# Performance work log

Measured on AMD Instinct MI355X. Metric: run time of the kernel, lower is better.

The kernel has to match this reference:

```python
import jax, jax.numpy as jnp
import numpy as np

# The torch module expresses conv as unfold -> linear (no bias) -> fold(1x1).
# That pipeline is mathematically exactly a VALID cross-correlation with the
# Linear weight reshaped to OIHW (torch unfold flattens patches in (C, kh, kw)
# order, matching Linear's in_features layout). We implement it as the
# efficient direct conv, which computes identical math.

B = 2048

def setup_inputs() -> dict:
    key = jax.random.key(0)
    k1, k2, k3 = jax.random.split(key, 3)
    x = jax.random.normal(k1, (B, 784), dtype=jnp.float32)
    # nn.Linear(49 -> 10, bias=False) and nn.Linear(250 -> 10, bias=False)
    W1 = jax.random.normal(k2, (10, 49), dtype=jnp.float32) * (1.0 / np.sqrt(49.0))
    W2 = jax.random.normal(k3, (10, 250), dtype=jnp.float32) * (1.0 / np.sqrt(250.0))
    return {"x": x, "W1": W1, "W2": W2}

def _conv(x, w_oihw):
    return jax.lax.conv_general_dilated(
        x, w_oihw, window_strides=(1, 1), padding='VALID',
        dimension_numbers=('NCHW', 'OIHW', 'NCHW'))

def _relu_ratio(x_base):
    # x = relu(x_base); ratio = x / x_base with NaN/Inf -> 0 (matches
    # calculate_ratio: 0/0 -> NaN -> 0, relu(neg)/neg -> -0 -> stays 0)
    x = jax.nn.relu(x_base)
    rat = x / x_base
    rat = jnp.where(jnp.isnan(rat) | jnp.isinf(rat), jnp.float32(0.0), rat)
    return x, rat

def reference(x, W1, W2):
    b = x.shape[0]
    h = x.reshape(b, 1, 28, 28)
    # layer 1: unfold(7x7) + linear(49->10) + fold == conv, out (b,10,22,22)
    h = _conv(h, W1.reshape(10, 1, 7, 7))
    h, rat1 = _relu_ratio(h)
    # layer 2: unfold(5x5) + linear(250->10) + fold == conv, out (b,10,18,18)
    h = _conv(h, W2.reshape(10, 10, 5, 5))
    h, rat2 = _relu_ratio(h)
    return (h, rat1, rat2)
```

## Files before the change

### kernel.cpp

```cpp
#include <hip/hip_runtime.h>


#define THREADS 256

__global__ __launch_bounds__(THREADS, 4) void brewcnn_v6(
    const float* __restrict__ x,
    const float* __restrict__ Wa,
    const float* __restrict__ Wb,
    float* __restrict__ out,
    int nimg)
{
    __shared__ __align__(16) float s_x[784];
    __shared__ __align__(16) float s_h[10 * 532];
    __shared__ __align__(16) float s_wa[492];
    __shared__ __align__(16) float s_wb[2840];
    const int img = blockIdx.x;
    const int tid = threadIdx.x;

    if (tid < 196)
        reinterpret_cast<float4*>(s_x)[tid] =
            reinterpret_cast<const float4*>(x + img * 784)[tid];
    if (tid < 122)
        reinterpret_cast<float4*>(s_wa)[tid] =
            reinterpret_cast<const float4*>(Wa)[tid];
    if (tid == 196) { s_wa[488] = Wa[488]; s_wa[489] = Wa[489]; }
    for (int t = tid; t < 2500; t += THREADS) {
        const int oc  = t / 250;
        const int rem = t - oc * 250;
        const int ic  = rem / 25;
        const int k   = rem - ic * 25;
        s_wb[oc * 284 + ic * 28 + k] = Wb[t];
    }
    __syncthreads();

    const int h2_base = img * 3240;
    const int r1_base = nimg * 3240 + img * 4840;
    const int r2_base = nimg * 8080 + img * 3240;

    {
        const int t   = tid < 220 ? tid : 219;
        const int row = t / 10;
        const int oc  = t - row * 10;

        float acc[22];
#pragma unroll
        for (int i = 0; i < 22; ++i) acc[i] = 0.0f;

        const float* wrow = s_wa + oc * 49;
#pragma unroll 1
        for (int ky = 0; ky < 7; ++ky) {
            float in[28];
            const float4* rp = reinterpret_cast<const float4*>(s_x + (row + ky) * 28);
#pragma unroll
            for (int j = 0; j < 7; ++j) {
                const float4 v = rp[j];
                in[4*j+0] = v.x; in[4*j+1] = v.y; in[4*j+2] = v.z; in[4*j+3] = v.w;
            }
            float w[7];
#pragma unroll
            for (int k = 0; k < 7; ++k) w[k] = wrow[ky * 7 + k];
#pragma unroll
            for (int kx = 0; kx < 7; ++kx)
#pragma unroll
                for (int px = 0; px < 22; ++px)
                    acc[px] = fmaf(in[px + kx], w[kx], acc[px]);
        }

        float r1v[22];
#pragma unroll
        for (int px = 0; px < 22; ++px) {
            const float h = acc[px];
            acc[px] = h > 0.0f ? h : 0.0f;
            r1v[px] = h > 0.0f ? 1.0f : 0.0f;
        }
        float* hdst = s_h + oc * 532 + row * 24;
#pragma unroll
        for (int j = 0; j < 5; ++j)
            reinterpret_cast<float4*>(hdst)[j] =
                make_float4(acc[4*j], acc[4*j+1], acc[4*j+2], acc[4*j+3]);
        hdst[20] = acc[20];
        hdst[21] = acc[21];

        float* r1p = out + r1_base + oc * 484 + row * 22;
#pragma unroll
        for (int j = 0; j < 11; ++j)
            reinterpret_cast<float2*>(r1p)[j] = make_float2(r1v[2*j], r1v[2*j+1]);
    }
    __syncthreads();

    {
        const int t   = tid < 180 ? tid : 179;
        const int row = t / 10;
        const int oc  = t - row * 10;

        float acc[18];
#pragma unroll
        for (int i = 0; i < 18; ++i) acc[i] = 0.0f;

#pragma unroll 1
        for (int ic = 0; ic < 10; ++ic) {
            float w[28];
            const float4* wp = reinterpret_cast<const float4*>(s_wb + oc * 284 + ic * 28);
#pragma unroll
            for (int j = 0; j < 7; ++j) {
                const float4 v = wp[j];
                w[4*j+0] = v.x; w[4*j+1] = v.y; w[4*j+2] = v.z; w[4*j+3] = v.w;
            }
            const float* hb = s_h + ic * 532 + row * 24;
#pragma unroll
            for (int ky = 0; ky < 5; ++ky) {
                float in[24];
                const float4* rp = reinterpret_cast<const float4*>(hb + ky * 24);
#pragma unroll
                for (int j = 0; j < 6; ++j) {
                    const float4 v = rp[j];
                    in[4*j+0] = v.x; in[4*j+1] = v.y; in[4*j+2] = v.z; in[4*j+3] = v.w;
                }
#pragma unroll
                for (int kx = 0; kx < 5; ++kx)
#pragma unroll
                    for (int px = 0; px < 18; ++px)
                        acc[px] = fmaf(in[px + kx], w[ky * 5 + kx], acc[px]);
            }
        }

        float hv[18], rv[18];
#pragma unroll
        for (int px = 0; px < 18; ++px) {
            const float h = acc[px];
            hv[px] = h > 0.0f ? h : 0.0f;
            rv[px] = h > 0.0f ? 1.0f : 0.0f;
        }
        float* h2p = out + h2_base + oc * 324 + row * 18;
        float* r2p = out + r2_base + oc * 324 + row * 18;
#pragma unroll
        for (int j = 0; j < 9; ++j) {
            reinterpret_cast<float2*>(h2p)[j] = make_float2(hv[2*j], hv[2*j+1]);
            reinterpret_cast<float2*>(r2p)[j] = make_float2(rv[2*j], rv[2*j+1]);
        }
    }
}

extern "C" void kernel_launch(void* const* d_in, const int* in_sizes, int n_in,
                              void* d_out, int out_size, void* d_ws, size_t ws_size,
                              hipStream_t stream) {
    const float* x  = (const float*)d_in[0];
    const float* Wa = (const float*)d_in[1];
    const float* Wb = (const float*)d_in[2];
    float* out = (float*)d_out;
    const int nimg = in_sizes[0] / 784;

    brewcnn_v6<<<nimg, THREADS, 0, stream>>>(x, Wa, Wb, out, nimg);
}
```

Baseline: 179.7 us.

## Compute multiple output rows per thread to reuse input rows across conv layers

```diff
diff --git a/kernel.cpp b/kernel.cpp
--- a/kernel.cpp
+++ b/kernel.cpp
@@ -1,9 +1,9 @@
 #include <hip/hip_runtime.h>
 
 
-#define THREADS 256
-
-__global__ __launch_bounds__(THREADS, 4) void brewcnn_v6(
+#define THREADS 128
+
+__global__ __launch_bounds__(THREADS) void brewcnn_v7(
     const float* __restrict__ x,
     const float* __restrict__ Wa,
     const float* __restrict__ Wb,
@@ -12,24 +12,21 @@
 {
     __shared__ __align__(16) float s_x[784];
     __shared__ __align__(16) float s_h[10 * 532];
-    __shared__ __align__(16) float s_wa[492];
-    __shared__ __align__(16) float s_wb[2840];
+    __shared__ __align__(16) float s_wa[560];
+    __shared__ __align__(16) float s_wb[2800];
     const int img = blockIdx.x;
     const int tid = threadIdx.x;
 
-    if (tid < 196)
-        reinterpret_cast<float4*>(s_x)[tid] =
-            reinterpret_cast<const float4*>(x + img * 784)[tid];
-    if (tid < 122)
-        reinterpret_cast<float4*>(s_wa)[tid] =
-            reinterpret_cast<const float4*>(Wa)[tid];
-    if (tid == 196) { s_wa[488] = Wa[488]; s_wa[489] = Wa[489]; }
-    for (int t = tid; t < 2500; t += THREADS) {
-        const int oc  = t / 250;
-        const int rem = t - oc * 250;
-        const int ic  = rem / 25;
-        const int k   = rem - ic * 25;
-        s_wb[oc * 284 + ic * 28 + k] = Wb[t];
+    for (int i = tid; i < 196; i += THREADS)
+        reinterpret_cast<float4*>(s_x)[i] =
+            reinterpret_cast<const float4*>(x + img * 784)[i];
+    for (int i = tid; i < 560; i += THREADS) {
+        const int oc = i / 56, r = i - oc * 56, ky = r >> 3, k = r & 7;
+        s_wa[i] = (k < 7) ? Wa[oc * 49 + ky * 7 + k] : 0.0f;
+    }
+    for (int i = tid; i < 2800; i += THREADS) {
+        const int oc = i / 280, r = i - oc * 280, ic = r / 28, k = r - ic * 28;
+        s_wb[i] = (k < 25) ? Wb[oc * 250 + ic * 25 + k] : 0.0f;
     }
     __syncthreads();
 
@@ -38,105 +35,171 @@
     const int r2_base = nimg * 8080 + img * 3240;
 
     {
-        const int t   = tid < 220 ? tid : 219;
-        const int row = t / 10;
-        const int oc  = t - row * 10;
-
-        float acc[22];
-#pragma unroll
-        for (int i = 0; i < 22; ++i) acc[i] = 0.0f;
-
-        const float* wrow = s_wa + oc * 49;
-#pragma unroll 1
-        for (int ky = 0; ky < 7; ++ky) {
-            float in[28];
-            const float4* rp = reinterpret_cast<const float4*>(s_x + (row + ky) * 28);
+        const int t  = tid < 110 ? tid : 109;
+        const int g  = t / 10;
+        const int oc = t - g * 10;
+        const int r0 = 2 * g;
+
+        float acc[2][22];
+#pragma unroll
+        for (int o = 0; o < 2; ++o)
+#pragma unroll
+            for (int px = 0; px < 22; ++px) acc[o][px] = 0.0f;
+
+        float wcur[7], wprev[7];
+        float in[28];
+
+        {
+            const float4* rp = reinterpret_cast<const float4*>(s_x + r0 * 28);
 #pragma unroll
             for (int j = 0; j < 7; ++j) {
                 const float4 v = rp[j];
                 in[4*j+0] = v.x; in[4*j+1] = v.y; in[4*j+2] = v.z; in[4*j+3] = v.w;
             }
-            float w[7];
-#pragma unroll
-            for (int k = 0; k < 7; ++k) w[k] = wrow[ky * 7 + k];
+            const float4* wp = reinterpret_cast<const float4*>(s_wa + oc * 56);
+            const float4 a = wp[0], b = wp[1];
+            wcur[0]=a.x; wcur[1]=a.y; wcur[2]=a.z; wcur[3]=a.w;
+            wcur[4]=b.x; wcur[5]=b.y; wcur[6]=b.z;
 #pragma unroll
             for (int kx = 0; kx < 7; ++kx)
 #pragma unroll
                 for (int px = 0; px < 22; ++px)
-                    acc[px] = fmaf(in[px + kx], w[kx], acc[px]);
-        }
-
-        float r1v[22];
-#pragma unroll
-        for (int px = 0; px < 22; ++px) {
-            const float h = acc[px];
-            acc[px] = h > 0.0f ? h : 0.0f;
-            r1v[px] = h > 0.0f ? 1.0f : 0.0f;
-        }
-        float* hdst = s_h + oc * 532 + row * 24;
+                    acc[0][px] = fmaf(in[px + kx], wcur[kx], acc[0][px]);
+#pragma unroll
+            for (int k = 0; k < 7; ++k) wprev[k] = wcur[k];
+        }
+
+#pragma unroll 1
+        for (int ri = 1; ri <= 6; ++ri) {
+            const float4* rp = reinterpret_cast<const float4*>(s_x + (r0 + ri) * 28);
+#pragma unroll
+            for (int j = 0; j < 7; ++j) {
+                const float4 v = rp[j];
+                in[4*j+0] = v.x; in[4*j+1] = v.y; in[4*j+2] = v.z; in[4*j+3] = v.w;
+            }
+            const float4* wp = reinterpret_cast<const float4*>(s_wa + oc * 56 + ri * 8);
+            const float4 a = wp[0], b = wp[1];
+            wcur[0]=a.x; wcur[1]=a.y; wcur[2]=a.z; wcur[3]=a.w;
+            wcur[4]=b.x; wcur[5]=b.y; wcur[6]=b.z;
+#pragma unroll
+            for (int kx = 0; kx < 7; ++kx)
+#pragma unroll
+                for (int px = 0; px < 22; ++px) {
+                    acc[0][px] = fmaf(in[px + kx], wcur[kx], acc[0][px]);
+                    acc[1][px] = fmaf(in[px + kx], wprev[kx], acc[1][px]);
+                }
+#pragma unroll
+            for (int k = 0; k < 7; ++k) wprev[k] = wcur[k];
+        }
+
+        {
+            const float4* rp = reinterpret_cast<const float4*>(s_x + (r0 + 7) * 28);
+#pragma unroll
+            for (int j = 0; j < 7; ++j) {
+                const float4 v = rp[j];
+                in[4*j+0] = v.x; in[4*j+1] = v.y; in[4*j+2] = v.z; in[4*j+3] = v.w;
+            }
+#pragma unroll
+            for (int kx = 0; kx < 7; ++kx)
+#pragma unroll
+                for (int px = 0; px < 22; ++px)
+                    acc[1][px] = fmaf(in[px + kx], wprev[kx], acc[1][px]);
+        }
+
+        float h[2][22], r[2][22];
+#pragma unroll
+        for (int o = 0; o < 2; ++o)
+#pragma unroll
+            for (int px = 0; px < 22; ++px) {
+                const float v = acc[o][px];
+                h[o][px] = v > 0.0f ? v : 0.0f;
+                r[o][px] = v > 0.0f ? 1.0f : 0.0f;
+            }
+        float4* hd = reinterpret_cast<float4*>(s_h + oc * 532 + r0 * 24);
 #pragma unroll
         for (int j = 0; j < 5; ++j)
-            reinterpret_cast<float4*>(hdst)[j] =
-                make_float4(acc[4*j], acc[4*j+1], acc[4*j+2], acc[4*j+3]);
-        hdst[20] = acc[20];
-        hdst[21] = acc[21];
-
-        float* r1p = out + r1_base + oc * 484 + row * 22;
-#pragma unroll
-        for (int j = 0; j < 11; ++j)
-            reinterpret_cast<float2*>(r1p)[j] = make_float2(r1v[2*j], r1v[2*j+1]);
+            hd[j] = make_float4(h[0][4*j], h[0][4*j+1], h[0][4*j+2], h[0][4*j+3]);
+        hd[5] = make_float4(h[0][20], h[0][21], 0.0f, 0.0f);
+#pragma unroll
+        for (int j = 0; j < 5; ++j)
+            hd[6 + j] = make_float4(h[1][4*j], h[1][4*j+1], h[1][4*j+2], h[1][4*j+3]);
+        hd[11] = make_float4(h[1][20], h[1][21], 0.0f, 0.0f);
+
+        float4* rp1 = reinterpret_cast<float4*>(out + r1_base + oc * 484 + r0 * 22);
+#pragma unroll
+        for (int j = 0; j < 11; ++j) {
+            const int base = 4 * j;
+            float v[4];
+#pragma unroll
+            for (int q = 0; q < 4; ++q) {
+                const int idx = base + q;
+                v[q] = (idx < 22) ? r[0][idx] : r[1][idx - 22];
+            }
+            rp1[j] = make_float4(v[0], v[1], v[2], v[3]);
+        }
     }
     __syncthreads();
 
-    {
-        const int t   = tid < 180 ? tid : 179;
-        const int row = t / 10;
-        const int oc  = t - row * 10;
-
-        float acc[18];
-#pragma unroll
-        for (int i = 0; i < 18; ++i) acc[i] = 0.0f;
+    if (tid < 64) {
+        const int t  = tid < 60 ? tid : 59;
+        const int g  = t / 10;
+        const int oc = t - g * 10;
+        const int r0 = 3 * g;
+
+        float acc[3][18];
+#pragma unroll
+        for (int o = 0; o < 3; ++o)
+#pragma unroll
+            for (int px = 0; px < 18; ++px) acc[o][px] = 0.0f;
 
 #pragma unroll 1
         for (int ic = 0; ic < 10; ++ic) {
             float w[28];
-            const float4* wp = reinterpret_cast<const float4*>(s_wb + oc * 284 + ic * 28);
+            const float4* wp = reinterpret_cast<const float4*>(s_wb + oc * 280 + ic * 28);
 #pragma unroll
             for (int j = 0; j < 7; ++j) {
                 const float4 v = wp[j];
                 w[4*j+0] = v.x; w[4*j+1] = v.y; w[4*j+2] = v.z; w[4*j+3] = v.w;
             }
-            const float* hb = s_h + ic * 532 + row * 24;
-#pragma unroll
-            for (int ky = 0; ky < 5; ++ky) {
+            const float* hb = s_h + ic * 532 + r0 * 24;
+#pragma unroll
+            for (int ri = 0; ri < 7; ++ri) {
                 float in[24];
-                const float4* rp = reinterpret_cast<const float4*>(hb + ky * 24);
+                const float4* rp = reinterpret_cast<const float4*>(hb + ri * 24);
 #pragma unroll
                 for (int j = 0; j < 6; ++j) {
                     const float4 v = rp[j];
                     in[4*j+0] = v.x; in[4*j+1] = v.y; in[4*j+2] = v.z; in[4*j+3] = v.w;
                 }
 #pragma unroll
-                for (int kx = 0; kx < 5; ++kx)
-#pragma unroll
-                    for (int px = 0; px < 18; ++px)
-                        acc[px] = fmaf(in[px + kx], w[ky * 5 + kx], acc[px]);
-            }
-        }
-
-        float hv[18], rv[18];
-#pragma unroll
-        for (int px = 0; px < 18; ++px) {
-            const float h = acc[px];
-            hv[px] = h > 0.0f ? h : 0.0f;
-            rv[px] = h > 0.0f ? 1.0f : 0.0f;
-        }
-        float* h2p = out + h2_base + oc * 324 + row * 18;
-        float* r2p = out + r2_base + oc * 324 + row * 18;
-#pragma unroll
-        for (int j = 0; j < 9; ++j) {
-            reinterpret_cast<float2*>(h2p)[j] = make_float2(hv[2*j], hv[2*j+1]);
-            reinterpret_cast<float2*>(r2p)[j] = make_float2(rv[2*j], rv[2*j+1]);
+                for (int o = 0; o < 3; ++o) {
+                    const int ky = ri - o;
+                    if (ky >= 0 && ky <= 4) {
+#pragma unroll
+                        for (int kx = 0; kx < 5; ++kx)
+#pragma unroll
+                            for (int px = 0; px < 18; ++px)
+                                acc[o][px] = fmaf(in[px + kx], w[ky * 5 + kx], acc[o][px]);
+                    }
+                }
+            }
+        }
+
+        float hv[54], rv[54];
+#pragma unroll
+        for (int o = 0; o < 3; ++o)
+#pragma unroll
+            for (int px = 0; px < 18; ++px) {
+                const float v = acc[o][px];
+                hv[o * 18 + px] = v > 0.0f ? v : 0.0f;
+                rv[o * 18 + px] = v > 0.0f ? 1.0f : 0.0f;
+            }
+        float2* h2p = reinterpret_cast<float2*>(out + h2_base + oc * 324 + r0 * 18);
+        float2* r2p = reinterpret_cast<float2*>(out + r2_base + oc * 324 + r0 * 18);
+#pragma unroll
+        for (int j = 0; j < 27; ++j) {
+            h2p[j] = make_float2(hv[2*j], hv[2*j+1]);
+            r2p[j] = make_float2(rv[2*j], rv[2*j+1]);
         }
     }
 }
@@ -150,5 +213,5 @@
     float* out = (float*)d_out;
     const int nimg = in_sizes[0] / 784;
 
-    brewcnn_v6<<<nimg, THREADS, 0, stream>>>(x, Wa, Wb, out, nimg);
+    brewcnn_v7<<<nimg, THREADS, 0, stream>>>(x, Wa, Wb, out, nimg);
 }
```

After: 192.4 us. 7.1% more time.
